# Performance work log

Hardware: AMD Instinct MI355X
Metric: run time of the kernel (lower is better)

Reference implementation:

```python
import jax, jax.numpy as jnp
import numpy as np

L, B, T, F, C, H, DFF = 2, 4, 2048, 1024, 200, 8, 128


def setup_inputs() -> dict:
    key = jax.random.key(0)
    ks = jax.random.split(key, 12)
    s = 0.02
    return {
        "x": jax.random.normal(ks[0], (B, T, F), jnp.float32),
        "prototypes": jax.random.normal(ks[1], (C, 1, F), jnp.float32),
        # conv_query / conv_key (1x1 convs == linear), per RAB layer
        "wq": jax.random.normal(ks[2], (L, F, F), jnp.float32) * s,
        "bq": jnp.zeros((L, F), jnp.float32),
        "wk": jax.random.normal(ks[3], (L, F, F), jnp.float32) * s,
        "bk": jnp.zeros((L, F), jnp.float32),
        # nn.MultiheadAttention packed in-proj and out-proj
        "in_w": jax.random.normal(ks[4], (L, 3 * F, F), jnp.float32) * s,
        "in_b": jnp.zeros((L, 3 * F), jnp.float32),
        "out_w": jax.random.normal(ks[5], (L, F, F), jnp.float32) * s,
        "out_b": jnp.zeros((L, F), jnp.float32),
        # FFN
        "l1_w": jax.random.normal(ks[6], (L, DFF, F), jnp.float32) * s,
        "l1_b": jnp.zeros((L, DFF), jnp.float32),
        "l2_w": jax.random.normal(ks[7], (L, F, DFF), jnp.float32) * s,
        "l2_b": jnp.zeros((L, F), jnp.float32),
        # LayerNorms
        "ln1_g": jnp.ones((L, F), jnp.float32),
        "ln1_b": jnp.zeros((L, F), jnp.float32),
        "ln2_g": jnp.ones((L, F), jnp.float32),
        "ln2_b": jnp.zeros((L, F), jnp.float32),
        # feature_embedding: Conv1d(F, F, k=3, pad=1) + ReLU
        "emb_w": jax.random.normal(ks[8], (F, F, 3), jnp.float32) * s,
        "emb_b": jnp.zeros((F,), jnp.float32),
    }


def _ln(x, g, b, eps=1e-5):
    mu = jnp.mean(x, axis=-1, keepdims=True)
    var = jnp.mean((x - mu) ** 2, axis=-1, keepdims=True)
    return (x - mu) * jax.lax.rsqrt(var + eps) * g + b


def _mha(q, k, v, w, b, ow, ob):
    # q,k,v: (B,S,F). Packed in-proj like nn.MultiheadAttention (eval: no dropout).
    f = q.shape[-1]
    dh = f // H
    Q = q @ w[:f].T + b[:f]
    K = k @ w[f:2 * f].T + b[f:2 * f]
    V = v @ w[2 * f:].T + b[2 * f:]
    sp = lambda t: t.reshape(t.shape[0], t.shape[1], H, dh)
    scale = np.float32(1.0 / np.sqrt(dh))
    att = jnp.einsum('bqhd,bkhd->bhqk', sp(Q), sp(K)) * scale
    att = jax.nn.softmax(att, axis=-1)
    o = jnp.einsum('bhqk,bkhd->bqhd', att, sp(V)).reshape(q.shape)
    return o @ ow.T + ob


def reference(x, prototypes, wq, bq, wk, bk, in_w, in_b, out_w, out_b,
              l1_w, l1_b, l2_w, l2_b, ln1_g, ln1_b, ln2_g, ln2_b, emb_w, emb_b):
    Bn, Tn, Fn = x.shape
    # torch: prototypes.view(1, F, -1)  (a reshape, NOT a transpose)
    proto = jnp.broadcast_to(prototypes.reshape(1, Fn, -1), (Bn, Fn, prototypes.shape[0]))
    # concat along time: (B,F,S) with S = T + C, then work in (B,S,F)
    src = jnp.swapaxes(jnp.concatenate([jnp.swapaxes(x, 1, 2), proto], axis=2), 1, 2)
    for l in range(L):
        q = src @ wq[l].T + bq[l]          # conv1x1 == pointwise linear
        k = src @ wk[l].T + bk[l]
        a = _mha(q, k, src, in_w[l], in_b[l], out_w[l], out_b[l])
        src = _ln(src + a, ln1_g[l], ln1_b[l])
        ff = jax.nn.relu(src @ l1_w[l].T + l1_b[l]) @ l2_w[l].T + l2_b[l]
        src = _ln(src + ff, ln2_g[l], ln2_b[l])
    feat = jnp.swapaxes(src[:, :Tn], 1, 2)  # (B,F,T): drop prototype tokens
    y = jax.lax.conv_general_dilated(feat, emb_w, (1,), ((1, 1),),
                                     dimension_numbers=('NCH', 'OIH', 'NCH'))
    return jax.nn.relu(y + emb_b[None, :, None])
```

## Files before the change

kernel.cpp:

```cpp
#include <hip/hip_runtime.h>
#include <hip/hip_bf16.h>


constexpr int BN = 4, TN = 2048, FD = 1024, CP = 200, SN = TN + CP;
constexpr int HN = 8, DH = 128, DF = 128, MR = BN * SN;
constexpr int SF = 3 * FD;
constexpr int NT = (SN + 63) / 64;
constexpr float C2 = 0.12751744f;

typedef __attribute__((ext_vector_type(8))) short short8;
typedef __attribute__((ext_vector_type(4))) float f32x4;

__device__ __forceinline__ ushort f2b(float f) {
  union { float f; uint u; } v{f};
  return (ushort)((v.u + 0x7fffu + ((v.u >> 16) & 1u)) >> 16);
}
__device__ __forceinline__ float b2f(ushort u) {
  union { uint u; float f; } v{(uint)u << 16};
  return v.f;
}
__device__ __forceinline__ uint cvt_pk_bf16(float a, float b) {
  uint r;
  asm("v_cvt_pk_bf16_f32 %0, %1, %2" : "=v"(r) : "v"(a), "v"(b));
  return r;
}
__device__ __forceinline__ float exp2_fast(float x) {
  float r;
  asm("v_exp_f32 %0, %1" : "=v"(r) : "v"(x));
  return r;
}
__device__ __forceinline__ void gld16(const void* g, void* l) {
  __builtin_amdgcn_global_load_lds(
      (const __attribute__((address_space(1))) void*)g,
      (__attribute__((address_space(3))) void*)l, 16, 0, 0);
}

__global__ __launch_bounds__(256) void k_build(const float* __restrict__ x,
                                               const float* __restrict__ proto,
                                               ushort* __restrict__ srcb) {
  const int row = blockIdx.x;
  const int b = row / SN, s = row % SN;
  const int f = threadIdx.x * 4;
  const size_t o = (size_t)row * FD + f;
  float4 v;
  if (s < TN) {
    v = *(const float4*)(x + ((size_t)b * TN + s) * FD + f);
  } else {
    const int c = s - TN;
    v.x = proto[(size_t)(f + 0) * CP + c];
    v.y = proto[(size_t)(f + 1) * CP + c];
    v.z = proto[(size_t)(f + 2) * CP + c];
    v.w = proto[(size_t)(f + 3) * CP + c];
  }
  ushort4 u{f2b(v.x), f2b(v.y), f2b(v.z), f2b(v.w)};
  *(ushort4*)(srcb + o) = u;
}

__global__ __launch_bounds__(256) void k_cvt(const float* __restrict__ in,
                                             ushort* __restrict__ out, int n) {
  const int n4 = n >> 2;
  for (int i = blockIdx.x * 256 + threadIdx.x; i < n4; i += gridDim.x * 256) {
    const float4 v = *(const float4*)(in + (size_t)i * 4);
    ushort4 u{f2b(v.x), f2b(v.y), f2b(v.z), f2b(v.w)};
    *(ushort4*)(out + (size_t)i * 4) = u;
  }
}

__global__ __launch_bounds__(256) void k_cvtT(const float* __restrict__ Wg,
                                              ushort* __restrict__ WTg) {
  const float* W = Wg + (size_t)blockIdx.z * FD * FD;
  ushort* WT = WTg + (size_t)blockIdx.z * FD * FD;
  __shared__ float t[32][33];
  const int tx = threadIdx.x & 31, ty = threadIdx.x >> 5;
  const int x0 = blockIdx.x * 32, y0 = blockIdx.y * 32;
#pragma unroll
  for (int dy = 0; dy < 4; ++dy)
    t[ty + dy * 8][tx] = W[(size_t)(y0 + ty + dy * 8) * FD + x0 + tx];
  __syncthreads();
#pragma unroll
  for (int dy = 0; dy < 4; ++dy)
    WT[(size_t)(x0 + ty + dy * 8) * FD + y0 + tx] = f2b(t[tx][ty + dy * 8]);
}

__global__ __launch_bounds__(256) void k_vT(const ushort* __restrict__ V,
                                            ushort* __restrict__ Vt) {
  __shared__ ushort t[32][34];
  const int tx = threadIdx.x & 31, ty = threadIdx.x >> 5;
  const int s0 = blockIdx.x * 32, d0 = blockIdx.y * 32, bh = blockIdx.z;
  const int b = bh >> 3, h = bh & 7;
#pragma unroll
  for (int dy = 0; dy < 4; ++dy) {
    const int s = min(s0 + ty + dy * 8, SN - 1);
    t[ty + dy * 8][tx] = V[((size_t)b * SN + s) * SF + h * DH + d0 + tx];
  }
  __syncthreads();
#pragma unroll
  for (int dy = 0; dy < 4; ++dy) {
    const int s = s0 + tx;
    if (s < SN)
      Vt[((size_t)bh * DH + d0 + ty + dy * 8) * SN + s] = t[tx][ty + dy * 8];
  }
}

__global__ __launch_bounds__(256) void k_convw(const float* __restrict__ W,
                                               ushort* __restrict__ out) {
  const int n = FD * FD * 3;
  for (int idx = blockIdx.x * 256 + threadIdx.x; idx < n;
       idx += gridDim.x * 256) {
    const int o = idx / (FD * 3);
    const int rem = idx % (FD * 3);
    const int tau = rem >> 10, i = rem & 1023;
    out[idx] = f2b(W[(size_t)o * (FD * 3) + i * 3 + tau]);
  }
}

__global__ __launch_bounds__(256) void k_pad(const ushort* __restrict__ sb,
                                             ushort* __restrict__ pad) {
  const int r = blockIdx.x, b = blockIdx.y;
  const int f = threadIdx.x * 4;
  ushort4 v{0, 0, 0, 0};
  if (r >= 1 && r <= TN)
    v = *(const ushort4*)(sb + ((size_t)b * SN + (r - 1)) * FD + f);
  *(ushort4*)(pad + ((size_t)b * (TN + 2) + r) * FD + f) = v;
}

__global__ __launch_bounds__(256) void k_beff(const float* __restrict__ in_w,
                                              const float* __restrict__ bvec,
                                              const float* __restrict__ in_b,
                                              float* __restrict__ out, int qk) {
  const int n = blockIdx.x, l = blockIdx.y, tid = threadIdx.x;
  const float* Win = in_w + (size_t)(l * 3 + qk) * FD * FD;
  const float* bv = bvec + (size_t)l * FD;
  float s = 0.f;
  for (int j = tid; j < FD; j += 256) s += Win[(size_t)n * FD + j] * bv[j];
  __shared__ float red[4];
#pragma unroll
  for (int o = 32; o; o >>= 1) s += __shfl_xor(s, o);
  if ((tid & 63) == 0) red[tid >> 6] = s;
  __syncthreads();
  if (tid == 0)
    out[l * 3 * FD + qk * FD + n] =
        red[0] + red[1] + red[2] + red[3] + in_b[l * 3 * FD + qk * FD + n];
}

__global__ __launch_bounds__(256) void k_copyv(const float* __restrict__ in_b,
                                               float* __restrict__ bqkv) {
  const int l = blockIdx.y;
  const int i = blockIdx.x * 256 + threadIdx.x;
  bqkv[l * 3 * FD + 2 * FD + i] = in_b[l * 3 * FD + 2 * FD + i];
}

template <bool RELU, bool BF16OUT>
__global__ __launch_bounds__(256) void k_mm(const ushort* __restrict__ A,
                                            const ushort* __restrict__ W,
                                            const float* __restrict__ bias,
                                            void* __restrict__ Cv,
                                            int M, int N, int K) {
  __shared__ __align__(16) ushort As[128 * 32];
  __shared__ __align__(16) ushort Ws[128 * 32];
  const int tid = threadIdx.x;
  const int lane = tid & 63, wv = tid >> 6;
  const int l15 = lane & 15, g = lane >> 4;
  const int wr = wv >> 1, wc = wv & 1;
  int bx = blockIdx.x, by = blockIdx.y;
  const int nwg = gridDim.x * gridDim.y;
  if ((nwg & 7) == 0) {
    int bid = by * gridDim.x + bx;
    bid = (bid & 7) * (nwg >> 3) + (bid >> 3);
    bx = bid % gridDim.x;
    by = bid / gridDim.x;
  }
  const int m0 = by * 128, n0 = bx * 128;
  f32x4 acc[4][4];
#pragma unroll
  for (int i = 0; i < 4; ++i)
#pragma unroll
    for (int j = 0; j < 4; ++j) acc[i][j] = (f32x4){0.f, 0.f, 0.f, 0.f};

  for (int k0 = 0; k0 < K; k0 += 32) {
#pragma unroll
    for (int j = 0; j < 2; ++j) {
      const int u = j * 256 + wv * 64 + lane;
      const int r = u >> 2, c = (u & 3) * 8;
      const int gm = min(m0 + r, M - 1);
      gld16(A + (size_t)gm * K + k0 + c, As + (size_t)u * 8);
    }
#pragma unroll
    for (int j = 0; j < 2; ++j) {
      const int u = j * 256 + wv * 64 + lane;
      const int r = u >> 2, c = (u & 3) * 8;
      gld16(W + (size_t)(n0 + r) * K + k0 + c, Ws + (size_t)u * 8);
    }
    __syncthreads();
    short8 af[4], bfr[4];
#pragma unroll
    for (int i = 0; i < 4; ++i)
      af[i] = *(const short8*)(As + (wr * 64 + i * 16 + l15) * 32 + g * 8);
#pragma unroll
    for (int j = 0; j < 4; ++j)
      bfr[j] = *(const short8*)(Ws + (wc * 64 + j * 16 + l15) * 32 + g * 8);
    __builtin_amdgcn_s_setprio(1);
#pragma unroll
    for (int i = 0; i < 4; ++i)
#pragma unroll
      for (int j = 0; j < 4; ++j)
        acc[i][j] = __builtin_amdgcn_mfma_f32_16x16x32_bf16(af[i], bfr[j],
                                                            acc[i][j], 0, 0, 0);
    __builtin_amdgcn_s_setprio(0);
    __syncthreads();
  }
#pragma unroll
  for (int i = 0; i < 4; ++i) {
#pragma unroll
    for (int r = 0; r < 4; ++r) {
      const int row = m0 + wr * 64 + i * 16 + g * 4 + r;
      if (row >= M) continue;
#pragma unroll
      for (int j = 0; j < 4; ++j) {
        const int col = n0 + wc * 64 + j * 16 + l15;
        float v = acc[i][j][r];
        if (bias) v += bias[col];
        if (RELU) v = fmaxf(v, 0.f);
        if (BF16OUT)
          ((ushort*)Cv)[(size_t)row * N + col] = f2b(v);
        else
          ((float*)Cv)[(size_t)row * N + col] = v;
      }
    }
  }
}

template <bool CONV, bool BF16OUT>
__global__ __launch_bounds__(512, 1) void k_mmB(const ushort* __restrict__ A,
                                                const ushort* __restrict__ W,
                                                const float* __restrict__ bias,
                                                void* __restrict__ Cv,
                                                int M, int N, int K) {
  __shared__ __align__(16) ushort As[2][128 * 64];
  __shared__ __align__(16) ushort Bs[2][256 * 64];
  const int tid = threadIdx.x;
  const int lane = tid & 63, wv = tid >> 6;
  const int l15 = lane & 15, g = lane >> 4;
  const int wr = wv >> 2, wc = wv & 3;
  int bx = blockIdx.x, by = blockIdx.y;
  const int nwg = gridDim.x * gridDim.y;
  if ((nwg & 7) == 0) {
    int bid = by * gridDim.x + bx;
    bid = (bid & 7) * (nwg >> 3) + (bid >> 3);
    bx = bid % gridDim.x;
    by = bid / gridDim.x;
  }
  const int m0 = by * 128, n0 = bx * 256;
  const int NKt = K >> 6;

  f32x4 acc[4][4];
#pragma unroll
  for (int i = 0; i < 4; ++i)
#pragma unroll
    for (int j = 0; j < 4; ++j) acc[i][j] = (f32x4){0.f, 0.f, 0.f, 0.f};

  auto stage = [&](int kt, int d) {
    const int kb = kt * 64;
#pragma unroll
    for (int j = 0; j < 2; ++j) {
      const int u = j * 512 + tid;
      const int row = u >> 3, s = u & 7;
      const int c = s ^ (row & 7);
      const ushort* ga;
      if (CONV) {
        const int rm = m0 + row;
        const int bb = rm >> 11, tt = rm & 2047;
        ga = A + (size_t)(bb * (TN + 2) + tt + (kb >> 10)) * FD + (kb & 1023) +
             c * 8;
      } else {
        ga = A + (size_t)min(m0 + row, M - 1) * K + kb + c * 8;
      }
      gld16(ga, As[d] + row * 64 + s * 8);
    }
#pragma unroll
    for (int j = 0; j < 4; ++j) {
      const int u = j * 512 + tid;
      const int row = u >> 3, s = u & 7;
      const int c = s ^ (row & 7);
      gld16(W + (size_t)(n0 + row) * K + kb + c * 8, Bs[d] + row * 64 + s * 8);
    }
  };

  stage(0, 0);
  for (int kt = 0; kt < NKt; ++kt) {
    const int cur = kt & 1;
    if (kt + 1 < NKt) {
      stage(kt + 1, cur ^ 1);
      asm volatile("s_waitcnt vmcnt(6)" ::: "memory");
    } else {
      asm volatile("s_waitcnt vmcnt(0)" ::: "memory");
    }
    __builtin_amdgcn_s_barrier();
    __builtin_amdgcn_sched_barrier(0);
#pragma unroll
    for (int ks = 0; ks < 2; ++ks) {
      short8 aq[4], bq[4];
#pragma unroll
      for (int mf = 0; mf < 4; ++mf) {
        const int row = wr * 64 + mf * 16 + l15;
        aq[mf] = *(const short8*)(As[cur] + row * 64 +
                                  (((ks * 4 + g) ^ (row & 7)) << 3));
      }
#pragma unroll
      for (int nf = 0; nf < 4; ++nf) {
        const int row = wc * 64 + nf * 16 + l15;
        bq[nf] = *(const short8*)(Bs[cur] + row * 64 +
                                  (((ks * 4 + g) ^ (row & 7)) << 3));
      }
      __builtin_amdgcn_s_setprio(1);
#pragma unroll
      for (int mf = 0; mf < 4; ++mf)
#pragma unroll
        for (int nf = 0; nf < 4; ++nf)
          acc[mf][nf] = __builtin_amdgcn_mfma_f32_16x16x32_bf16(
              aq[mf], bq[nf], acc[mf][nf], 0, 0, 0);
      __builtin_amdgcn_s_setprio(0);
    }
    asm volatile("s_waitcnt lgkmcnt(0)" ::: "memory");
    __builtin_amdgcn_s_barrier();
  }

#pragma unroll
  for (int mf = 0; mf < 4; ++mf) {
#pragma unroll
    for (int r = 0; r < 4; ++r) {
      const int row = m0 + wr * 64 + mf * 16 + g * 4 + r;
      if (!CONV && row >= M) continue;
#pragma unroll
      for (int nf = 0; nf < 4; ++nf) {
        const int col = n0 + wc * 64 + nf * 16 + l15;
        float v = acc[mf][nf][r];
        if (bias) v += bias[col];
        if (CONV) {
          v = fmaxf(v, 0.f);
          const int bb = row >> 11, tt = row & 2047;
          ((float*)Cv)[((size_t)(bb * FD + col)) * TN + tt] = v;
        } else if (BF16OUT) {
          ((ushort*)Cv)[(size_t)row * N + col] = f2b(v);
        } else {
          ((float*)Cv)[(size_t)row * N + col] = v;
        }
      }
    }
  }
}

__global__ __launch_bounds__(256) void k_fattn(const ushort* __restrict__ Qg,
                                               const ushort* __restrict__ Kg,
                                               const ushort* __restrict__ Vt,
                                               ushort* __restrict__ Og) {
  __shared__ __align__(16) ushort Ks[64 * 128];
  __shared__ __align__(16) ushort Vs[128 * 64];
  __shared__ __align__(16) ushort Ps[4][16 * 64];
  const int tid = threadIdx.x, lane = tid & 63, wv = tid >> 6;
  const int l15 = lane & 15, g = lane >> 4;
  const int b = blockIdx.z, h = blockIdx.y, q0 = blockIdx.x * 64;
  const size_t rowBase = (size_t)b * SN;
  const int hoff = h * DH;
  const size_t vbase = (size_t)(b * HN + h) * DH * SN;

  short8 qf[4];
  const int qrow = min(q0 + wv * 16 + l15, SN - 1);
#pragma unroll
  for (int c = 0; c < 4; ++c)
    qf[c] = *(const short8*)(Qg + (rowBase + qrow) * SF + hoff + c * 32 + g * 8);

  short8 onesf;
#pragma unroll
  for (int i = 0; i < 8; ++i) onesf[i] = (short)0x3F80;

  f32x4 o[8];
#pragma unroll
  for (int dt = 0; dt < 8; ++dt) o[dt] = (f32x4){0.f, 0.f, 0.f, 0.f};
  f32x4 lacc = (f32x4){0.f, 0.f, 0.f, 0.f};
  const char* KsB = (const char*)Ks;
  const char* VsB = (const char*)Vs;
  char* PsB = (char*)&Ps[wv][0];

  for (int t = 0; t < NT; ++t) {
    const int kv0 = t * 64;
    const bool tl = (t == NT - 1);
    if (tl) {
#pragma unroll
      for (int j = 0; j < 4; ++j) {
        const int su = j * 256 + tid;
        const int row = su >> 4, s = su & 15;
        const int c16 = s ^ (row & 7);
        const int krow = min(kv0 + row, SN - 1);
        gld16(Kg + (rowBase + krow) * SF + hoff + c16 * 8, Ks + (size_t)su * 8);
      }
#pragma unroll
      for (int j = 0; j < 4; ++j) {
        const int su = j * 256 + tid;
        const int row = su >> 3, s = su & 7;
        const int cc = s ^ (row & 7);
        const int kvc = min(kv0 + cc * 8, SN - 8);
        gld16(Vt + vbase + (size_t)row * SN + kvc, Vs + (size_t)su * 8);
      }
    } else {
#pragma unroll
      for (int j = 0; j < 4; ++j) {
        const int su = j * 256 + tid;
        const int row = su >> 4, s = su & 15;
        const int c16 = s ^ (row & 7);
        gld16(Kg + (rowBase + kv0 + row) * SF + hoff + c16 * 8,
              Ks + (size_t)su * 8);
      }
#pragma unroll
      for (int j = 0; j < 4; ++j) {
        const int su = j * 256 + tid;
        const int row = su >> 3, s = su & 7;
        const int cc = s ^ (row & 7);
        gld16(Vt + vbase + (size_t)row * SN + kv0 + cc * 8,
              Vs + (size_t)su * 8);
      }
    }
    __syncthreads();

    f32x4 st[4];
    __builtin_amdgcn_s_setprio(1);
#pragma unroll
    for (int kt = 0; kt < 4; ++kt) {
      f32x4 s4 = (f32x4){0.f, 0.f, 0.f, 0.f};
      const int row = kt * 16 + l15;
#pragma unroll
      for (int c = 0; c < 4; ++c) {
        const short8 kf = *(const short8*)(
            KsB + row * 256 + (((c * 4 + g) ^ (row & 7)) << 4));
        s4 = __builtin_amdgcn_mfma_f32_16x16x32_bf16(kf, qf[c], s4, 0, 0, 0);
      }
      st[kt] = s4;
    }
    __builtin_amdgcn_s_setprio(0);

    float pfl[16];
    if (tl) {
#pragma unroll
      for (int kt = 0; kt < 4; ++kt)
#pragma unroll
        for (int r = 0; r < 4; ++r) {
          const int kvg = kv0 + kt * 16 + g * 4 + r;
          pfl[kt * 4 + r] = (kvg < SN) ? exp2_fast(C2 * st[kt][r]) : 0.f;
        }
    } else {
#pragma unroll
      for (int i = 0; i < 16; ++i)
        pfl[i] = exp2_fast(C2 * st[i >> 2][i & 3]);
    }

#pragma unroll
    for (int kt = 0; kt < 4; ++kt) {
      const uint lo = cvt_pk_bf16(pfl[kt * 4 + 0], pfl[kt * 4 + 1]);
      const uint hi = cvt_pk_bf16(pfl[kt * 4 + 2], pfl[kt * 4 + 3]);
      const int slot = (kt * 2 + (g >> 1)) ^ (l15 & 7);
      *(uint2*)(PsB + l15 * 128 + slot * 16 + (g & 1) * 8) = make_uint2(lo, hi);
    }

    __builtin_amdgcn_s_setprio(1);
#pragma unroll
    for (int c2 = 0; c2 < 2; ++c2) {
      const int pslot = (c2 * 4 + g) ^ (l15 & 7);
      const short8 pf = *(const short8*)(PsB + l15 * 128 + pslot * 16);
      lacc = __builtin_amdgcn_mfma_f32_16x16x32_bf16(pf, onesf, lacc, 0, 0, 0);
#pragma unroll
      for (int dt = 0; dt < 8; ++dt) {
        const int row = dt * 16 + l15;
        const short8 vf = *(const short8*)(
            VsB + row * 128 + (((c2 * 4 + g) ^ (row & 7)) << 4));
        o[dt] = __builtin_amdgcn_mfma_f32_16x16x32_bf16(pf, vf, o[dt], 0, 0, 0);
      }
    }
    __builtin_amdgcn_s_setprio(0);
    __syncthreads();
  }

  float ir[4];
#pragma unroll
  for (int r = 0; r < 4; ++r) ir[r] = 1.f / lacc[r];
#pragma unroll
  for (int r = 0; r < 4; ++r) {
    const int orow = q0 + wv * 16 + g * 4 + r;
    if (orow >= SN) continue;
#pragma unroll
    for (int dt = 0; dt < 8; ++dt)
      Og[(rowBase + orow) * FD + hoff + dt * 16 + l15] = f2b(o[dt][r] * ir[r]);
  }
}

__global__ __launch_bounds__(256) void k_add_ln(ushort* __restrict__ sb,
                                                const ushort* __restrict__ d,
                                                const float* __restrict__ g,
                                                const float* __restrict__ be) {
  __shared__ float red[4];
  const int row = blockIdx.x;
  const int tid = threadIdx.x;
  const int c = tid * 4;
  const size_t off = (size_t)row * FD + c;
  const ushort4 sv = *(const ushort4*)(sb + off);
  const ushort4 dv = *(const ushort4*)(d + off);
  float v[4] = {b2f(sv.x) + b2f(dv.x), b2f(sv.y) + b2f(dv.y),
                b2f(sv.z) + b2f(dv.z), b2f(sv.w) + b2f(dv.w)};
  float sum = v[0] + v[1] + v[2] + v[3];
#pragma unroll
  for (int o = 32; o; o >>= 1) sum += __shfl_xor(sum, o);
  if ((tid & 63) == 0) red[tid >> 6] = sum;
  __syncthreads();
  sum = red[0] + red[1] + red[2] + red[3];
  const float mu = sum * (1.f / FD);
  float vs = 0.f;
#pragma unroll
  for (int i = 0; i < 4; ++i) {
    const float t = v[i] - mu;
    vs += t * t;
  }
  __syncthreads();
#pragma unroll
  for (int o = 32; o; o >>= 1) vs += __shfl_xor(vs, o);
  if ((tid & 63) == 0) red[tid >> 6] = vs;
  __syncthreads();
  vs = red[0] + red[1] + red[2] + red[3];
  const float rstd = rsqrtf(vs * (1.f / FD) + 1e-5f);
  const float4 gv = *(const float4*)(g + c);
  const float4 bv = *(const float4*)(be + c);
  ushort4 u{f2b((v[0] - mu) * rstd * gv.x + bv.x),
            f2b((v[1] - mu) * rstd * gv.y + bv.y),
            f2b((v[2] - mu) * rstd * gv.z + bv.z),
            f2b((v[3] - mu) * rstd * gv.w + bv.w)};
  *(ushort4*)(sb + off) = u;
}

extern "C" void kernel_launch(void* const* d_in, const int* in_sizes, int n_in,
                              void* d_out, int out_size, void* d_ws,
                              size_t ws_size, hipStream_t stream) {
  const float* x      = (const float*)d_in[0];
  const float* proto  = (const float*)d_in[1];
  const float* wq     = (const float*)d_in[2];
  const float* bq     = (const float*)d_in[3];
  const float* wk     = (const float*)d_in[4];
  const float* bk     = (const float*)d_in[5];
  const float* in_w   = (const float*)d_in[6];
  const float* in_b   = (const float*)d_in[7];
  const float* out_w  = (const float*)d_in[8];
  const float* out_b  = (const float*)d_in[9];
  const float* l1_w   = (const float*)d_in[10];
  const float* l1_b   = (const float*)d_in[11];
  const float* l2_w   = (const float*)d_in[12];
  const float* l2_b   = (const float*)d_in[13];
  const float* ln1_g  = (const float*)d_in[14];
  const float* ln1_b  = (const float*)d_in[15];
  const float* ln2_g  = (const float*)d_in[16];
  const float* ln2_b  = (const float*)d_in[17];
  const float* emb_w  = (const float*)d_in[18];
  const float* emb_b  = (const float*)d_in[19];

  char* p = (char*)d_ws;
  auto take = [&](size_t bytes) {
    char* r = p;
    p += (bytes + 255) & ~(size_t)255;
    return r;
  };
  const size_t MF = (size_t)MR * FD;
  const size_t FF = (size_t)FD * FD;
  ushort* srcb  = (ushort*)take(MF * 2);
  ushort* bQKV  = (ushort*)take((size_t)MR * SF * 2);
  ushort* bVt   = (ushort*)take((size_t)BN * HN * DH * SN * 2);
  ushort* bO    = (ushort*)take(MF * 2);
  ushort* bFF   = (ushort*)take((size_t)MR * DF * 2);
  ushort* wQKV  = (ushort*)take((size_t)2 * 3 * FF * 2);
  ushort* wOut  = (ushort*)take((size_t)2 * FF * 2);
  ushort* wL1   = (ushort*)take((size_t)2 * DF * FD * 2);
  ushort* wL2   = (ushort*)take((size_t)2 * FD * DF * 2);
  float*  bqkv  = (float*)take((size_t)2 * SF * 4);
  ushort* wT     = bQKV;
  ushort* wInQK  = bQKV + 4 * FF;
  ushort* bOut   = bQKV;
  ushort* srcPad = bQKV;
  ushort* convW  = bQKV + (size_t)10 * 1024 * 1024;

  k_build<<<MR, 256, 0, stream>>>(x, proto, srcb);
  k_cvt<<<1024, 256, 0, stream>>>(in_w, wInQK, 2 * FF);
  k_cvt<<<1024, 256, 0, stream>>>(in_w + 3 * FF, wInQK + 2 * FF, 2 * FF);
  k_cvt<<<1024, 256, 0, stream>>>(in_w + 2 * FF, wQKV + 2 * FF, FF);
  k_cvt<<<1024, 256, 0, stream>>>(in_w + 5 * FF, wQKV + 5 * FF, FF);
  k_cvt<<<1024, 256, 0, stream>>>(out_w, wOut, 2 * FF);
  k_cvt<<<256, 256, 0, stream>>>(l1_w, wL1, 2 * DF * FD);
  k_cvt<<<256, 256, 0, stream>>>(l2_w, wL2, 2 * FD * DF);
  k_cvtT<<<dim3(32, 32, 2), 256, 0, stream>>>(wq, wT);
  k_cvtT<<<dim3(32, 32, 2), 256, 0, stream>>>(wk, wT + 2 * FF);
  for (int l = 0; l < 2; ++l)
    for (int qk = 0; qk < 2; ++qk)
      k_mm<false, true><<<dim3(8, 8), 256, 0, stream>>>(
          wInQK + (size_t)(l * 2 + qk) * FF, wT + (size_t)(qk * 2 + l) * FF,
          nullptr, wQKV + (size_t)(l * 3 + qk) * FF, FD, FD, FD);
  k_beff<<<dim3(FD, 2), 256, 0, stream>>>(in_w, bq, in_b, bqkv, 0);
  k_beff<<<dim3(FD, 2), 256, 0, stream>>>(in_w, bk, in_b, bqkv, 1);
  k_copyv<<<dim3(4, 2), 256, 0, stream>>>(in_b, bqkv);

  const int MB = (MR + 127) / 128;

  for (int l = 0; l < 2; ++l) {
    k_mmB<false, true><<<dim3(SF / 256, MB), 512, 0, stream>>>(
        srcb, wQKV + (size_t)l * 3 * FF, bqkv + (size_t)l * SF, bQKV, MR, SF,
        FD);
    k_vT<<<dim3((SN + 31) / 32, DH / 32, BN * HN), 256, 0, stream>>>(
        bQKV + 2 * FD, bVt);
    k_fattn<<<dim3((SN + 63) / 64, HN, BN), 256, 0, stream>>>(
        bQKV, bQKV + FD, bVt, bO);
    k_mmB<false, true><<<dim3(FD / 256, MB), 512, 0, stream>>>(
        bO, wOut + (size_t)l * FF, out_b + (size_t)l * FD, bOut, MR, FD, FD);
    k_add_ln<<<MR, 256, 0, stream>>>(srcb, bOut, ln1_g + (size_t)l * FD,
                                     ln1_b + (size_t)l * FD);
    k_mm<true, true><<<dim3(DF / 128, MB), 256, 0, stream>>>(
        srcb, wL1 + (size_t)l * DF * FD, l1_b + (size_t)l * DF, bFF, MR, DF,
        FD);
    k_mm<false, true><<<dim3(FD / 128, MB), 256, 0, stream>>>(
        bFF, wL2 + (size_t)l * FD * DF, l2_b + (size_t)l * FD, bOut, MR, FD,
        DF);
    k_add_ln<<<MR, 256, 0, stream>>>(srcb, bOut, ln2_g + (size_t)l * FD,
                                     ln2_b + (size_t)l * FD);
  }

  k_convw<<<1024, 256, 0, stream>>>(emb_w, convW);
  k_pad<<<dim3(TN + 2, BN), 256, 0, stream>>>(srcb, srcPad);
  k_mmB<true, false><<<dim3(FD / 256, (BN * TN) / 128), 512, 0, stream>>>(
      srcPad, convW, emb_b, (float*)d_out, BN * TN, FD, 3 * FD);
}
```

Baseline: 1.049 ms.

## Enlarge attention blocks to 128 queries and batch weight-prep launches

The flash-attention kernel now runs 512 threads (8 waves) per block over 128 query rows, so each K/V tile loaded into shared memory serves twice as many queries, halving K/V global traffic per query. Separately, the four in_w conversion launches become one kernel, the two transposes one launch, and the four Q/K weight-fusion GEMMs one batched launch via blockIdx.z, cutting launch overhead. The tradeoff is fewer attention blocks (144 vs 288 per layer's grid), which may reduce occupancy or latency hiding on 256 CUs, plus more shared memory and registers per block.

Result: faster. 0.9997 ms (-4.7%).

```diff
diff --git a/kernel.cpp b/kernel.cpp
--- a/kernel.cpp
+++ b/kernel.cpp
@@ -66,10 +66,30 @@
   }
 }
 
-__global__ __launch_bounds__(256) void k_cvtT(const float* __restrict__ Wg,
-                                              ushort* __restrict__ WTg) {
-  const float* W = Wg + (size_t)blockIdx.z * FD * FD;
-  ushort* WT = WTg + (size_t)blockIdx.z * FD * FD;
+__global__ __launch_bounds__(256) void k_cvt_inw(const float* __restrict__ in,
+                                                 ushort* __restrict__ wInQK,
+                                                 ushort* __restrict__ wQKV) {
+  constexpr size_t FF = (size_t)FD * FD;
+  const int n4 = (int)(6 * FF / 4);
+  for (int i = blockIdx.x * 256 + threadIdx.x; i < n4; i += gridDim.x * 256) {
+    const size_t idx = (size_t)i * 4;
+    const float4 v = *(const float4*)(in + idx);
+    ushort4 u{f2b(v.x), f2b(v.y), f2b(v.z), f2b(v.w)};
+    const int l = (int)(idx / (3 * FF));
+    const size_t r = idx % (3 * FF);
+    ushort* dst = (r >= 2 * FF) ? (wQKV + l * 3 * FF + r)
+                                : (wInQK + l * 2 * FF + r);
+    *(ushort4*)dst = u;
+  }
+}
+
+__global__ __launch_bounds__(256) void k_cvtT(const float* __restrict__ wq,
+                                              const float* __restrict__ wk,
+                                              ushort* __restrict__ wT) {
+  const int z = blockIdx.z;
+  const int qk = z >> 1, l = z & 1;
+  const float* W = (qk ? wk : wq) + (size_t)l * FD * FD;
+  ushort* WT = wT + (size_t)z * FD * FD;
   __shared__ float t[32][33];
   const int tx = threadIdx.x & 31, ty = threadIdx.x >> 5;
   const int x0 = blockIdx.x * 32, y0 = blockIdx.y * 32;
@@ -150,12 +170,19 @@
   bqkv[l * 3 * FD + 2 * FD + i] = in_b[l * 3 * FD + 2 * FD + i];
 }
 
-template <bool RELU, bool BF16OUT>
+template <bool RELU, bool BF16OUT, bool PREP4 = false>
 __global__ __launch_bounds__(256) void k_mm(const ushort* __restrict__ A,
                                             const ushort* __restrict__ W,
                                             const float* __restrict__ bias,
                                             void* __restrict__ Cv,
                                             int M, int N, int K) {
+  constexpr size_t FF = (size_t)FD * FD;
+  if (PREP4) {
+    const int z = blockIdx.z;
+    A += (size_t)z * FF;
+    W += (size_t)(((z & 1) * 2) + (z >> 1)) * FF;
+    Cv = (void*)((ushort*)Cv + (size_t)((z >> 1) * 3 + (z & 1)) * FF);
+  }
   __shared__ __align__(16) ushort As[128 * 32];
   __shared__ __align__(16) ushort Ws[128 * 32];
   const int tid = threadIdx.x;
@@ -350,16 +377,16 @@
   }
 }
 
-__global__ __launch_bounds__(256) void k_fattn(const ushort* __restrict__ Qg,
+__global__ __launch_bounds__(512) void k_fattn(const ushort* __restrict__ Qg,
                                                const ushort* __restrict__ Kg,
                                                const ushort* __restrict__ Vt,
                                                ushort* __restrict__ Og) {
   __shared__ __align__(16) ushort Ks[64 * 128];
   __shared__ __align__(16) ushort Vs[128 * 64];
-  __shared__ __align__(16) ushort Ps[4][16 * 64];
+  __shared__ __align__(16) ushort Ps[8][16 * 64];
   const int tid = threadIdx.x, lane = tid & 63, wv = tid >> 6;
   const int l15 = lane & 15, g = lane >> 4;
-  const int b = blockIdx.z, h = blockIdx.y, q0 = blockIdx.x * 64;
+  const int b = blockIdx.z, h = blockIdx.y, q0 = blockIdx.x * 128;
   const size_t rowBase = (size_t)b * SN;
   const int hoff = h * DH;
   const size_t vbase = (size_t)(b * HN + h) * DH * SN;
@@ -387,16 +414,16 @@
     const bool tl = (t == NT - 1);
     if (tl) {
 #pragma unroll
-      for (int j = 0; j < 4; ++j) {
-        const int su = j * 256 + tid;
+      for (int j = 0; j < 2; ++j) {
+        const int su = j * 512 + tid;
         const int row = su >> 4, s = su & 15;
         const int c16 = s ^ (row & 7);
         const int krow = min(kv0 + row, SN - 1);
         gld16(Kg + (rowBase + krow) * SF + hoff + c16 * 8, Ks + (size_t)su * 8);
       }
 #pragma unroll
-      for (int j = 0; j < 4; ++j) {
-        const int su = j * 256 + tid;
+      for (int j = 0; j < 2; ++j) {
+        const int su = j * 512 + tid;
         const int row = su >> 3, s = su & 7;
         const int cc = s ^ (row & 7);
         const int kvc = min(kv0 + cc * 8, SN - 8);
@@ -404,16 +431,16 @@
       }
     } else {
 #pragma unroll
-      for (int j = 0; j < 4; ++j) {
-        const int su = j * 256 + tid;
+      for (int j = 0; j < 2; ++j) {
+        const int su = j * 512 + tid;
         const int row = su >> 4, s = su & 15;
         const int c16 = s ^ (row & 7);
         gld16(Kg + (rowBase + kv0 + row) * SF + hoff + c16 * 8,
               Ks + (size_t)su * 8);
       }
 #pragma unroll
-      for (int j = 0; j < 4; ++j) {
-        const int su = j * 256 + tid;
+      for (int j = 0; j < 2; ++j) {
+        const int su = j * 512 + tid;
         const int row = su >> 3, s = su & 7;
         const int cc = s ^ (row & 7);
         gld16(Vt + vbase + (size_t)row * SN + kv0 + cc * 8,
@@ -583,20 +610,13 @@
   ushort* convW  = bQKV + (size_t)10 * 1024 * 1024;
 
   k_build<<<MR, 256, 0, stream>>>(x, proto, srcb);
-  k_cvt<<<1024, 256, 0, stream>>>(in_w, wInQK, 2 * FF);
-  k_cvt<<<1024, 256, 0, stream>>>(in_w + 3 * FF, wInQK + 2 * FF, 2 * FF);
-  k_cvt<<<1024, 256, 0, stream>>>(in_w + 2 * FF, wQKV + 2 * FF, FF);
-  k_cvt<<<1024, 256, 0, stream>>>(in_w + 5 * FF, wQKV + 5 * FF, FF);
+  k_cvt_inw<<<2048, 256, 0, stream>>>(in_w, wInQK, wQKV);
   k_cvt<<<1024, 256, 0, stream>>>(out_w, wOut, 2 * FF);
   k_cvt<<<256, 256, 0, stream>>>(l1_w, wL1, 2 * DF * FD);
   k_cvt<<<256, 256, 0, stream>>>(l2_w, wL2, 2 * FD * DF);
-  k_cvtT<<<dim3(32, 32, 2), 256, 0, stream>>>(wq, wT);
-  k_cvtT<<<dim3(32, 32, 2), 256, 0, stream>>>(wk, wT + 2 * FF);
-  for (int l = 0; l < 2; ++l)
-    for (int qk = 0; qk < 2; ++qk)
-      k_mm<false, true><<<dim3(8, 8), 256, 0, stream>>>(
-          wInQK + (size_t)(l * 2 + qk) * FF, wT + (size_t)(qk * 2 + l) * FF,
-          nullptr, wQKV + (size_t)(l * 3 + qk) * FF, FD, FD, FD);
+  k_cvtT<<<dim3(32, 32, 4), 256, 0, stream>>>(wq, wk, wT);
+  k_mm<false, true, true><<<dim3(8, 8, 4), 256, 0, stream>>>(
+      wInQK, wT, nullptr, wQKV, FD, FD, FD);
   k_beff<<<dim3(FD, 2), 256, 0, stream>>>(in_w, bq, in_b, bqkv, 0);
   k_beff<<<dim3(FD, 2), 256, 0, stream>>>(in_w, bk, in_b, bqkv, 1);
   k_copyv<<<dim3(4, 2), 256, 0, stream>>>(in_b, bqkv);
@@ -609,7 +629,7 @@
         FD);
     k_vT<<<dim3((SN + 31) / 32, DH / 32, BN * HN), 256, 0, stream>>>(
         bQKV + 2 * FD, bVt);
-    k_fattn<<<dim3((SN + 63) / 64, HN, BN), 256, 0, stream>>>(
+    k_fattn<<<dim3((SN + 127) / 128, HN, BN), 512, 0, stream>>>(
         bQKV, bQKV + FD, bVt, bO);
     k_mmB<false, true><<<dim3(FD / 256, MB), 512, 0, stream>>>(
         bO, wOut + (size_t)l * FF, out_b + (size_t)l * FD, bOut, MR, FD, FD);
```
